# Kernel tuning notes

Measured on AMD Instinct MI355X. Metric: run time of the kernel, lower is better.

Reference implementation:

```python
import jax, jax.numpy as jnp
import numpy as np

B, S, H, NH, BS = 1, 4096, 1024, 16, 64  # batch, seq, hidden, heads, block_size
HD = H // NH                             # head_dim = 64
SPARSITY = 0.9


def _block_sparse_mask():
    # Mirrors SparseAttention._compute_block_mask: random block mask * upper-tri,
    # expanded by block_size. Diagonal blocks forced on so no row is fully masked.
    nb = S // BS
    rng = np.random.default_rng(0)
    keep = rng.random((nb, nb)) > SPARSITY
    tri = np.triu(np.ones((nb, nb), dtype=bool))
    bm = (keep & tri) | np.eye(nb, dtype=bool)
    full = np.repeat(np.repeat(bm, BS, axis=0), BS, axis=1)  # [S,S]
    return jnp.asarray(full[None, None])                     # [1,1,S,S]


def setup_inputs() -> dict:
    key = jax.random.key(0)
    ks = jax.random.split(key, 5)
    std = 0.02
    return {
        "hidden_states": jax.random.normal(ks[0], (B, S, H), dtype=jnp.float32),
        "wq": jax.random.normal(ks[1], (H, H), dtype=jnp.float32) * std,
        "bq": jnp.zeros((H,), dtype=jnp.float32),
        "wk": jax.random.normal(ks[2], (H, H), dtype=jnp.float32) * std,
        "bk": jnp.zeros((H,), dtype=jnp.float32),
        "wv": jax.random.normal(ks[3], (H, H), dtype=jnp.float32) * std,
        "bv": jnp.zeros((H,), dtype=jnp.float32),
        "wo": jax.random.normal(ks[4], (H, H), dtype=jnp.float32) * std,
        "bo": jnp.zeros((H,), dtype=jnp.float32),
        "attention_mask": _block_sparse_mask(),
    }


def reference(hidden_states, wq, bq, wk, bk, wv, bv, wo, bo, attention_mask):
    b, s, h = hidden_states.shape
    scaling = HD ** -0.5

    def split_heads(x):  # [B,S,H] -> [B,NH,S,HD]
        return x.reshape(b, s, NH, HD).transpose(0, 2, 1, 3)

    q = split_heads(hidden_states @ wq.T + bq)
    k = split_heads(hidden_states @ wk.T + bk)
    v = split_heads(hidden_states @ wv.T + bv)

    scores = jnp.einsum("bhqd,bhkd->bhqk", q, k) * scaling  # [B,NH,S,S]
    scores = jnp.where(attention_mask, scores, -jnp.inf)
    probs = jax.nn.softmax(scores, axis=-1)  # dropout is identity in eval
    attn = jnp.einsum("bhqk,bhkd->bhqd", probs, v)
    attn = attn.transpose(0, 2, 1, 3).reshape(b, s, h)
    return attn @ wo.T + bo
```

## Files before the change

kernel.cpp:

```cpp
#include <hip/hip_runtime.h>
#include <hip/hip_bf16.h>
#include <stdint.h>

#define SEQ   4096
#define HID   1024
#define NHEAD 16
#define HD    64
#define NBLK  64

typedef __bf16 bf16;
typedef __bf16 bf16x8 __attribute__((ext_vector_type(8)));
typedef __bf16 bf16x4 __attribute__((ext_vector_type(4)));
typedef float  floatx4 __attribute__((ext_vector_type(4)));

__device__ __forceinline__ void gl_lds16(const void* g, void* l) {
  __builtin_amdgcn_global_load_lds(
      (const __attribute__((address_space(1))) void*)g,
      (__attribute__((address_space(3))) void*)l, 16, 0, 0);
}

__device__ __forceinline__ int detect_f32(const void* p) {
  unsigned wv = ((const unsigned*)p)[threadIdx.x & 63];
  unsigned ex = ((wv & 0xFFFFu) >> 7) & 0xFFu;
  unsigned long long b = __ballot(ex >= 140u);
  return __popcll(b) >= 8;
}

__global__ void build_blocklist(const void* mask, int* cnt, int* list) {
  unsigned w0 = ((const unsigned*)mask)[0], w1 = ((const unsigned*)mask)[1];
  int f;
  if (w0 == 0x01010101u)                  f = 1;
  else if (w0 == 0x3F803F80u)             f = 2;
  else if (w0 == 0x3C003C00u)             f = 2;
  else if (w0 == 0x3F800000u)             f = 3;
  else if (w0 == 1u && w1 == 1u)          f = 0;
  else if (w0 == 1u && w1 == 0u)          f = 4;
  else if (w0 == 0u && w1 == 0x3FF00000u) f = 5;
  else f = 0;

  int i = blockIdx.x, j = threadIdx.x;
  size_t e = (size_t)i * 64 * SEQ + (size_t)j * 64;
  bool kept;
  switch (f) {
    case 1: kept = ((const unsigned char*)mask)[e] != 0; break;
    case 2: kept = ((const unsigned short*)mask)[e] != 0; break;
    case 3: kept = ((const unsigned*)mask)[e] != 0; break;
    case 4:
    case 5: kept = ((const unsigned long long*)mask)[e] != 0ull; break;
    default: kept = ((const int*)mask)[e] != 0; break;
  }
  unsigned long long b = __ballot(kept);
  if (kept) {
    int idx = __popcll(b & ((1ull << j) - 1ull));
    list[i * 64 + idx] = j;
  }
  if (j == 0) cnt[i] = (int)__popcll(b);
}

__global__ __launch_bounds__(256) void convert_inputs(
    const void* p0, const void* p1, const void* p2, const void* p3,
    const void* p4, const void* p5, const void* p6, const void* p7,
    const void* p8, bf16* dst)
{
  int f32 = detect_f32(p0);
  int tid = blockIdx.x * blockDim.x + threadIdx.x;
  const int TOT4 = 8392704 / 4;
  for (int q = tid; q < TOT4; q += gridDim.x * blockDim.x) {
    int e = q * 4;
    const void* src; int off;
    if      (e < 4194304) { src = p0; off = 0; }
    else if (e < 5242880) { src = p1; off = 4194304; }
    else if (e < 5243904) { src = p2; off = 5242880; }
    else if (e < 6292480) { src = p3; off = 5243904; }
    else if (e < 6293504) { src = p4; off = 6292480; }
    else if (e < 7342080) { src = p5; off = 6293504; }
    else if (e < 7343104) { src = p6; off = 7342080; }
    else if (e < 8391680) { src = p7; off = 7343104; }
    else                  { src = p8; off = 8391680; }
    int le = e - off;
    bf16x4 v;
    if (f32) {
      const float* s = (const float*)src + le;
      v[0] = (bf16)s[0]; v[1] = (bf16)s[1]; v[2] = (bf16)s[2]; v[3] = (bf16)s[3];
    } else {
      v = *(const bf16x4*)((const bf16*)src + le);
    }
    *(bf16x4*)(dst + e) = v;
  }
}

__device__ __forceinline__ void gemm128_body(
    const bf16* __restrict__ A, const bf16* __restrict__ Bw,
    const bf16* __restrict__ bias, void* __restrict__ Cout,
    float scale, int mode, int f32out, bf16* As, bf16* Bs)
{
  const int K = HID, N = HID;
  int bn = blockIdx.x, bm = blockIdx.y;
  int t = threadIdx.x;
  int w = t >> 6, lane = t & 63;
  int wm = w >> 1, wn = w & 1;
  int lr = lane & 15, lq = lane >> 4;

  floatx4 acc[4][4] = {};

  const bf16* Ab = A  + (size_t)bm * 128 * K;
  const bf16* Bb = Bw + (size_t)bn * 128 * K;

  for (int k0 = 0; k0 < K; k0 += 32) {
    __syncthreads();
#pragma unroll
    for (int p = 0; p < 2; ++p) {
      int ci = p * 256 + t;
      int row = ci >> 2, c8 = (ci & 3) * 8;
      gl_lds16(Ab + (size_t)row * K + k0 + c8, As + ci * 8);
      gl_lds16(Bb + (size_t)row * K + k0 + c8, Bs + ci * 8);
    }
    __syncthreads();

    bf16x8 af[4], bfv[4];
#pragma unroll
    for (int i = 0; i < 4; ++i) {
      af[i]  = *(const bf16x8*)(As + (wm * 64 + i * 16 + lr) * 32 + lq * 8);
      bfv[i] = *(const bf16x8*)(Bs + (wn * 64 + i * 16 + lr) * 32 + lq * 8);
    }
#pragma unroll
    for (int mi = 0; mi < 4; ++mi)
#pragma unroll
      for (int ni = 0; ni < 4; ++ni)
        acc[mi][ni] = __builtin_amdgcn_mfma_f32_16x16x32_bf16(
            af[mi], bfv[ni], acc[mi][ni], 0, 0, 0);
  }

#pragma unroll
  for (int mi = 0; mi < 4; ++mi)
#pragma unroll
    for (int ni = 0; ni < 4; ++ni) {
      int col = bn * 128 + wn * 64 + ni * 16 + lr;
      float bv = (float)bias[col];
      if (mode == 2) {
        int row0 = bm * 128 + wm * 64 + mi * 16 + lq * 4;
        bf16x4 pk;
#pragma unroll
        for (int r = 0; r < 4; ++r)
          pk[r] = (bf16)((acc[mi][ni][r] + bv) * scale);
        size_t off = (size_t)(col >> 6) * HD * SEQ + (size_t)(col & 63) * SEQ + row0;
        *(bf16x4*)((bf16*)Cout + off) = pk;
      } else {
#pragma unroll
        for (int r = 0; r < 4; ++r) {
          int row = bm * 128 + wm * 64 + mi * 16 + lq * 4 + r;
          float v = (acc[mi][ni][r] + bv) * scale;
          if (mode == 1)
            ((bf16*)Cout)[(size_t)(col >> 6) * SEQ * HD + (size_t)row * HD + (col & 63)] = (bf16)v;
          else if (f32out)
            ((float*)Cout)[(size_t)row * N + col] = v;
          else
            ((bf16*)Cout)[(size_t)row * N + col] = (bf16)v;
        }
      }
    }
}

__global__ __launch_bounds__(256) void gemm_qkv_kernel(
    const bf16* __restrict__ X,
    const bf16* __restrict__ wq, const bf16* __restrict__ wk, const bf16* __restrict__ wv,
    const bf16* __restrict__ bq, const bf16* __restrict__ bk, const bf16* __restrict__ bv,
    bf16* __restrict__ Q, bf16* __restrict__ K, bf16* __restrict__ Vt)
{
  __shared__ __align__(16) bf16 As[128 * 32];
  __shared__ __align__(16) bf16 Bs[128 * 32];
  int z = blockIdx.z;
  const bf16* W = (z == 0) ? wq : (z == 1) ? wk : wv;
  const bf16* b = (z == 0) ? bq : (z == 1) ? bk : bv;
  bf16* O = (z == 0) ? Q : (z == 1) ? K : Vt;
  float scale = (z == 0) ? 0.125f : 1.0f;
  int mode = (z == 2) ? 2 : 1;
  gemm128_body(X, W, b, O, scale, mode, 0, As, Bs);
}

__global__ __launch_bounds__(256) void gemm_out_kernel(
    const bf16* __restrict__ A, const bf16* __restrict__ W,
    const bf16* __restrict__ b, void* __restrict__ O, const void* hs_raw)
{
  __shared__ __align__(16) bf16 As[128 * 32];
  __shared__ __align__(16) bf16 Bs[128 * 32];
  int f32o = detect_f32(hs_raw);
  gemm128_body(A, W, b, O, 1.0f, 0, f32o, As, Bs);
}

__global__ __launch_bounds__(256) void sparse_attn(
    const bf16* __restrict__ Qh, const bf16* __restrict__ Kh,
    const bf16* __restrict__ Vt, const int* __restrict__ cnt,
    const int* __restrict__ list, bf16* __restrict__ attn_out)
{
  int qb = blockIdx.x, h = blockIdx.y;
  int t = threadIdx.x, w = t >> 6, lane = t & 63;
  int lr = lane & 15, lq = lane >> 4;

  __shared__ __align__(16) bf16 Ks[64 * 64];
  __shared__ __align__(16) bf16 Vs[64 * 64];
  __shared__ __align__(16) bf16 Pl[4 * 16 * 72];

  const bf16* Qbase = Qh + (size_t)h * SEQ * HD;
  const bf16* Kbase = Kh + (size_t)h * SEQ * HD;
  const bf16* Vtb   = Vt + (size_t)h * HD * SEQ;

  bf16x8 qf[2];
#pragma unroll
  for (int ks = 0; ks < 2; ++ks)
    qf[ks] = *(const bf16x8*)&Qbase[(size_t)(qb * 64 + w * 16 + lr) * HD + ks * 32 + lq * 8];

  floatx4 o_acc[4] = {};
  float l_lane[4] = {0.f, 0.f, 0.f, 0.f};

  int ciA = t, ciB = t + 256;
  int base = qb * 64;
  int n = cnt[qb];

  int kb = list[base];
  const bf16* Kb = Kbase + (size_t)kb * (64 * HD);
  bf16x8 kr0 = *(const bf16x8*)(Kb + ciA * 8);
  bf16x8 kr1 = *(const bf16x8*)(Kb + ciB * 8);
  bf16x8 vr0 = *(const bf16x8*)(Vtb + (size_t)(ciA >> 3) * SEQ + kb * 64 + (ciA & 7) * 8);
  bf16x8 vr1 = *(const bf16x8*)(Vtb + (size_t)(ciB >> 3) * SEQ + kb * 64 + (ciB & 7) * 8);

  bf16* Pw = Pl + w * 16 * 72;
  for (int it = 0; it < n; ++it) {
    *(bf16x8*)(Ks + ciA * 8) = kr0;
    *(bf16x8*)(Ks + ciB * 8) = kr1;
    *(bf16x8*)(Vs + ciA * 8) = vr0;
    *(bf16x8*)(Vs + ciB * 8) = vr1;
    __syncthreads();

    if (it + 1 < n) {
      int kb2 = list[base + it + 1];
      const bf16* Kb2 = Kbase + (size_t)kb2 * (64 * HD);
      kr0 = *(const bf16x8*)(Kb2 + ciA * 8);
      kr1 = *(const bf16x8*)(Kb2 + ciB * 8);
      vr0 = *(const bf16x8*)(Vtb + (size_t)(ciA >> 3) * SEQ + kb2 * 64 + (ciA & 7) * 8);
      vr1 = *(const bf16x8*)(Vtb + (size_t)(ciB >> 3) * SEQ + kb2 * 64 + (ciB & 7) * 8);
    }

    floatx4 s_acc[4] = {};
#pragma unroll
    for (int ks = 0; ks < 2; ++ks)
#pragma unroll
      for (int ni = 0; ni < 4; ++ni) {
        bf16x8 kf = *(const bf16x8*)&Ks[(ni * 16 + lr) * 64 + ks * 32 + lq * 8];
        s_acc[ni] = __builtin_amdgcn_mfma_f32_16x16x32_bf16(qf[ks], kf, s_acc[ni], 0, 0, 0);
      }

    float pvv[4][4];
#pragma unroll
    for (int ni = 0; ni < 4; ++ni)
#pragma unroll
      for (int r = 0; r < 4; ++r) {
        float p = __expf(s_acc[ni][r] - 3.0f);
        pvv[ni][r] = p;
        l_lane[r] += p;
      }

#pragma unroll
    for (int ni = 0; ni < 4; ++ni)
#pragma unroll
      for (int r = 0; r < 4; ++r)
        Pw[(lq * 4 + r) * 72 + ni * 16 + lr] = (bf16)pvv[ni][r];

#pragma unroll
    for (int ks = 0; ks < 2; ++ks) {
      bf16x8 pf = *(const bf16x8*)&Pw[lr * 72 + ks * 32 + lq * 8];
#pragma unroll
      for (int ni = 0; ni < 4; ++ni) {
        bf16x8 vf = *(const bf16x8*)&Vs[(ni * 16 + lr) * 64 + ks * 32 + lq * 8];
        o_acc[ni] = __builtin_amdgcn_mfma_f32_16x16x32_bf16(pf, vf, o_acc[ni], 0, 0, 0);
      }
    }
    __syncthreads();
  }

  float l_row[4];
#pragma unroll
  for (int r = 0; r < 4; ++r) {
    float s = l_lane[r];
#pragma unroll
    for (int d = 1; d < 16; d <<= 1) s += __shfl_xor(s, d, 64);
    l_row[r] = s;
  }

#pragma unroll
  for (int ni = 0; ni < 4; ++ni)
#pragma unroll
    for (int r = 0; r < 4; ++r) {
      int row = qb * 64 + w * 16 + lq * 4 + r;
      int col = h * 64 + ni * 16 + lr;
      attn_out[(size_t)row * HID + col] = (bf16)(o_acc[ni][r] / l_row[r]);
    }
}

extern "C" void kernel_launch(void* const* d_in, const int* in_sizes, int n_in,
                              void* d_out, int out_size, void* d_ws, size_t ws_size,
                              hipStream_t stream)
{
  const void* hs = d_in[0];
  const void* wq = d_in[1];
  const void* bq = d_in[2];
  const void* wk = d_in[3];
  const void* bk = d_in[4];
  const void* wv = d_in[5];
  const void* bv = d_in[6];
  const void* wo = d_in[7];
  const void* bo = d_in[8];
  const void* mask = d_in[9];

  char* ws = (char*)d_ws;
  const size_t SZ = (size_t)NHEAD * SEQ * HD;
  bf16* conv = (bf16*)ws;
  bf16* hs_b = conv;
  bf16* wq_b = conv + 4194304;
  bf16* bq_b = conv + 5242880;
  bf16* wk_b = conv + 5243904;
  bf16* bk_b = conv + 6292480;
  bf16* wv_b = conv + 6293504;
  bf16* bv_b = conv + 7342080;
  bf16* wo_b = conv + 7343104;
  bf16* bo_b = conv + 8391680;
  bf16* Q  = conv + 8392704;
  bf16* Kh = Q  + SZ;
  bf16* Vt = Kh + SZ;
  bf16* At = Vt + SZ;
  int* cnt  = (int*)(At + SZ);
  int* list = cnt + 64;

  convert_inputs<<<2048, 256, 0, stream>>>(hs, wq, bq, wk, bk, wv, bv, wo, bo, conv);
  build_blocklist<<<NBLK, 64, 0, stream>>>(mask, cnt, list);
  gemm_qkv_kernel<<<dim3(8, 32, 3), 256, 0, stream>>>(hs_b, wq_b, wk_b, wv_b,
                                                      bq_b, bk_b, bv_b, Q, Kh, Vt);
  sparse_attn<<<dim3(NBLK, NHEAD), 256, 0, stream>>>(Q, Kh, Vt, cnt, list, At);
  gemm_out_kernel<<<dim3(8, 32), 256, 0, stream>>>(At, wo_b, bo_b, d_out, hs);
}
```

Baseline: 238.5 us.

## Stage GEMM epilogue through LDS for coalesced stores, pad attention LDS tiles

The GEMM epilogue now stages each 16-row accumulator slice in shared memory and writes it out as vectorized row-contiguous stores, instead of scattered per-element stores. The V projection no longer writes a transposed layout directly. A separate transpose_v kernel builds Vt, using the At buffer as scratch before attention overwrites it. The attention kernel pads its K/V/P shared tiles to a 72-element row stride to cut LDS bank conflicts. These changes add an extra kernel launch, extra V traffic and extra barriers in the epilogue.

Result: faster. 231.7 us (-2.9%).

```diff
diff --git a/kernel.cpp b/kernel.cpp
--- a/kernel.cpp
+++ b/kernel.cpp
@@ -7,6 +7,7 @@
 #define NHEAD 16
 #define HD    64
 #define NBLK  64
+#define KSTR  72
 
 typedef __bf16 bf16;
 typedef __bf16 bf16x8 __attribute__((ext_vector_type(8)));
@@ -92,9 +93,11 @@
 __device__ __forceinline__ void gemm128_body(
     const bf16* __restrict__ A, const bf16* __restrict__ Bw,
     const bf16* __restrict__ bias, void* __restrict__ Cout,
-    float scale, int mode, int f32out, bf16* As, bf16* Bs)
+    float scale, int mode, int f32out, char* smem)
 {
   const int K = HID, N = HID;
+  bf16* As = (bf16*)smem;
+  bf16* Bs = (bf16*)(smem + 8192);
   int bn = blockIdx.x, bm = blockIdx.y;
   int t = threadIdx.x;
   int w = t >> 6, lane = t & 63;
@@ -131,61 +134,88 @@
             af[mi], bfv[ni], acc[mi][ni], 0, 0, 0);
   }
 
-#pragma unroll
-  for (int mi = 0; mi < 4; ++mi)
+  float* Ew = (float*)smem + w * 16 * 68;
+  int head = bn * 2 + wn;
+#pragma unroll
+  for (int mi = 0; mi < 4; ++mi) {
+    __syncthreads();
 #pragma unroll
     for (int ni = 0; ni < 4; ++ni) {
-      int col = bn * 128 + wn * 64 + ni * 16 + lr;
-      float bv = (float)bias[col];
-      if (mode == 2) {
-        int row0 = bm * 128 + wm * 64 + mi * 16 + lq * 4;
-        bf16x4 pk;
-#pragma unroll
-        for (int r = 0; r < 4; ++r)
-          pk[r] = (bf16)((acc[mi][ni][r] + bv) * scale);
-        size_t off = (size_t)(col >> 6) * HD * SEQ + (size_t)(col & 63) * SEQ + row0;
-        *(bf16x4*)((bf16*)Cout + off) = pk;
+      int colg = bn * 128 + wn * 64 + ni * 16 + lr;
+      float bv = (float)bias[colg];
+#pragma unroll
+      for (int r = 0; r < 4; ++r)
+        Ew[(lq * 4 + r) * 68 + ni * 16 + lr] = (acc[mi][ni][r] + bv) * scale;
+    }
+    __syncthreads();
+#pragma unroll
+    for (int hh = 0; hh < 4; ++hh) {
+      int s_loc = (lane >> 4) + hh * 4;
+      int c4 = (lane & 15) * 4;
+      floatx4 v = *(const floatx4*)&Ew[s_loc * 68 + c4];
+      int row = bm * 128 + wm * 64 + mi * 16 + s_loc;
+      if (mode == 1) {
+        bf16x4 pk; pk[0] = (bf16)v[0]; pk[1] = (bf16)v[1]; pk[2] = (bf16)v[2]; pk[3] = (bf16)v[3];
+        *(bf16x4*)&((bf16*)Cout)[(size_t)head * SEQ * HD + (size_t)row * HD + c4] = pk;
+      } else if (f32out) {
+        *(floatx4*)&((float*)Cout)[(size_t)row * N + bn * 128 + wn * 64 + c4] = v;
       } else {
-#pragma unroll
-        for (int r = 0; r < 4; ++r) {
-          int row = bm * 128 + wm * 64 + mi * 16 + lq * 4 + r;
-          float v = (acc[mi][ni][r] + bv) * scale;
-          if (mode == 1)
-            ((bf16*)Cout)[(size_t)(col >> 6) * SEQ * HD + (size_t)row * HD + (col & 63)] = (bf16)v;
-          else if (f32out)
-            ((float*)Cout)[(size_t)row * N + col] = v;
-          else
-            ((bf16*)Cout)[(size_t)row * N + col] = (bf16)v;
-        }
+        bf16x4 pk; pk[0] = (bf16)v[0]; pk[1] = (bf16)v[1]; pk[2] = (bf16)v[2]; pk[3] = (bf16)v[3];
+        *(bf16x4*)&((bf16*)Cout)[(size_t)row * N + bn * 128 + wn * 64 + c4] = pk;
       }
     }
+  }
 }
 
 __global__ __launch_bounds__(256) void gemm_qkv_kernel(
     const bf16* __restrict__ X,
     const bf16* __restrict__ wq, const bf16* __restrict__ wk, const bf16* __restrict__ wv,
     const bf16* __restrict__ bq, const bf16* __restrict__ bk, const bf16* __restrict__ bv,
-    bf16* __restrict__ Q, bf16* __restrict__ K, bf16* __restrict__ Vt)
-{
-  __shared__ __align__(16) bf16 As[128 * 32];
-  __shared__ __align__(16) bf16 Bs[128 * 32];
+    bf16* __restrict__ Q, bf16* __restrict__ K, bf16* __restrict__ Vh)
+{
+  __shared__ __align__(16) char smem[17408];
   int z = blockIdx.z;
   const bf16* W = (z == 0) ? wq : (z == 1) ? wk : wv;
   const bf16* b = (z == 0) ? bq : (z == 1) ? bk : bv;
-  bf16* O = (z == 0) ? Q : (z == 1) ? K : Vt;
+  bf16* O = (z == 0) ? Q : (z == 1) ? K : Vh;
   float scale = (z == 0) ? 0.125f : 1.0f;
-  int mode = (z == 2) ? 2 : 1;
-  gemm128_body(X, W, b, O, scale, mode, 0, As, Bs);
+  gemm128_body(X, W, b, O, scale, 1, 0, smem);
 }
 
 __global__ __launch_bounds__(256) void gemm_out_kernel(
     const bf16* __restrict__ A, const bf16* __restrict__ W,
     const bf16* __restrict__ b, void* __restrict__ O, const void* hs_raw)
 {
-  __shared__ __align__(16) bf16 As[128 * 32];
-  __shared__ __align__(16) bf16 Bs[128 * 32];
+  __shared__ __align__(16) char smem[17408];
   int f32o = detect_f32(hs_raw);
-  gemm128_body(A, W, b, O, 1.0f, 0, f32o, As, Bs);
+  gemm128_body(A, W, b, O, 1.0f, 0, f32o, smem);
+}
+
+__global__ __launch_bounds__(256) void transpose_v(
+    const bf16* __restrict__ Vh, bf16* __restrict__ Vt)
+{
+  int h = blockIdx.y, sb = blockIdx.x;
+  __shared__ __align__(16) bf16 T[64 * KSTR];
+  int t = threadIdx.x;
+  const bf16* Vb = Vh + (size_t)h * SEQ * HD + (size_t)sb * 64 * HD;
+#pragma unroll
+  for (int it = 0; it < 2; ++it) {
+    int s = (t >> 3) + it * 32;
+    int d0 = (t & 7) * 8;
+    bf16x8 v = *(const bf16x8*)&Vb[(size_t)s * HD + d0];
+#pragma unroll
+    for (int j = 0; j < 8; ++j)
+      T[(d0 + j) * KSTR + s] = v[j];
+  }
+  __syncthreads();
+  bf16* Vo = Vt + (size_t)h * HD * SEQ + (size_t)sb * 64;
+#pragma unroll
+  for (int it = 0; it < 2; ++it) {
+    int d = (t >> 3) + it * 32;
+    int s0 = (t & 7) * 8;
+    bf16x8 v = *(const bf16x8*)&T[d * KSTR + s0];
+    *(bf16x8*)&Vo[(size_t)d * SEQ + s0] = v;
+  }
 }
 
 __global__ __launch_bounds__(256) void sparse_attn(
@@ -197,9 +227,9 @@
   int t = threadIdx.x, w = t >> 6, lane = t & 63;
   int lr = lane & 15, lq = lane >> 4;
 
-  __shared__ __align__(16) bf16 Ks[64 * 64];
-  __shared__ __align__(16) bf16 Vs[64 * 64];
-  __shared__ __align__(16) bf16 Pl[4 * 16 * 72];
+  __shared__ __align__(16) bf16 Ks[64 * KSTR];
+  __shared__ __align__(16) bf16 Vs[64 * KSTR];
+  __shared__ __align__(16) bf16 Pl[4 * 16 * KSTR];
 
   const bf16* Qbase = Qh + (size_t)h * SEQ * HD;
   const bf16* Kbase = Kh + (size_t)h * SEQ * HD;
@@ -214,6 +244,8 @@
   float l_lane[4] = {0.f, 0.f, 0.f, 0.f};
 
   int ciA = t, ciB = t + 256;
+  int ofA = (ciA >> 3) * KSTR + (ciA & 7) * 8;
+  int ofB = (ciB >> 3) * KSTR + (ciB & 7) * 8;
   int base = qb * 64;
   int n = cnt[qb];
 
@@ -224,12 +256,12 @@
   bf16x8 vr0 = *(const bf16x8*)(Vtb + (size_t)(ciA >> 3) * SEQ + kb * 64 + (ciA & 7) * 8);
   bf16x8 vr1 = *(const bf16x8*)(Vtb + (size_t)(ciB >> 3) * SEQ + kb * 64 + (ciB & 7) * 8);
 
-  bf16* Pw = Pl + w * 16 * 72;
+  bf16* Pw = Pl + w * 16 * KSTR;
   for (int it = 0; it < n; ++it) {
-    *(bf16x8*)(Ks + ciA * 8) = kr0;
-    *(bf16x8*)(Ks + ciB * 8) = kr1;
-    *(bf16x8*)(Vs + ciA * 8) = vr0;
-    *(bf16x8*)(Vs + ciB * 8) = vr1;
+    *(bf16x8*)(Ks + ofA) = kr0;
+    *(bf16x8*)(Ks + ofB) = kr1;
+    *(bf16x8*)(Vs + ofA) = vr0;
+    *(bf16x8*)(Vs + ofB) = vr1;
     __syncthreads();
 
     if (it + 1 < n) {
@@ -246,7 +278,7 @@
     for (int ks = 0; ks < 2; ++ks)
 #pragma unroll
       for (int ni = 0; ni < 4; ++ni) {
-        bf16x8 kf = *(const bf16x8*)&Ks[(ni * 16 + lr) * 64 + ks * 32 + lq * 8];
+        bf16x8 kf = *(const bf16x8*)&Ks[(ni * 16 + lr) * KSTR + ks * 32 + lq * 8];
         s_acc[ni] = __builtin_amdgcn_mfma_f32_16x16x32_bf16(qf[ks], kf, s_acc[ni], 0, 0, 0);
       }
 
@@ -264,14 +296,14 @@
     for (int ni = 0; ni < 4; ++ni)
 #pragma unroll
       for (int r = 0; r < 4; ++r)
-        Pw[(lq * 4 + r) * 72 + ni * 16 + lr] = (bf16)pvv[ni][r];
+        Pw[(lq * 4 + r) * KSTR + ni * 16 + lr] = (bf16)pvv[ni][r];
 
 #pragma unroll
     for (int ks = 0; ks < 2; ++ks) {
-      bf16x8 pf = *(const bf16x8*)&Pw[lr * 72 + ks * 32 + lq * 8];
+      bf16x8 pf = *(const bf16x8*)&Pw[lr * KSTR + ks * 32 + lq * 8];
 #pragma unroll
       for (int ni = 0; ni < 4; ++ni) {
-        bf16x8 vf = *(const bf16x8*)&Vs[(ni * 16 + lr) * 64 + ks * 32 + lq * 8];
+        bf16x8 vf = *(const bf16x8*)&Vs[(ni * 16 + lr) * KSTR + ks * 32 + lq * 8];
         o_acc[ni] = __builtin_amdgcn_mfma_f32_16x16x32_bf16(pf, vf, o_acc[ni], 0, 0, 0);
       }
     }
@@ -328,13 +360,15 @@
   bf16* Kh = Q  + SZ;
   bf16* Vt = Kh + SZ;
   bf16* At = Vt + SZ;
+  bf16* Vh = At;
   int* cnt  = (int*)(At + SZ);
   int* list = cnt + 64;
 
   convert_inputs<<<2048, 256, 0, stream>>>(hs, wq, bq, wk, bk, wv, bv, wo, bo, conv);
   build_blocklist<<<NBLK, 64, 0, stream>>>(mask, cnt, list);
   gemm_qkv_kernel<<<dim3(8, 32, 3), 256, 0, stream>>>(hs_b, wq_b, wk_b, wv_b,
-                                                      bq_b, bk_b, bv_b, Q, Kh, Vt);
+                                                      bq_b, bk_b, bv_b, Q, Kh, Vh);
+  transpose_v<<<dim3(NBLK, NHEAD), 256, 0, stream>>>(Vh, Vt);
   sparse_attn<<<dim3(NBLK, NHEAD), 256, 0, stream>>>(Q, Kh, Vt, cnt, list, At);
   gemm_out_kernel<<<dim3(8, 32), 256, 0, stream>>>(At, wo_b, bo_b, d_out, hs);
 }
```
